# Optimization experiments

Measured on AMD Instinct MI355X. Metric: run time of the kernel, lower is better.

The kernel has to match this reference:

```python
import jax, jax.numpy as jnp
import numpy as np

DIM = 512
HEADS = 16
WS = (2, 7, 7)
N = WS[0] * WS[1] * WS[2]  # 98
NW = 64  # number of windows in mask
B_ = 512  # num_windows * batch
HEAD_DIM = DIM // HEADS
SCALE = HEAD_DIM ** -0.5
TABLE = (2 * WS[0] - 1) * (2 * WS[1] - 1) * (2 * WS[2] - 1)  # 507


def _relative_position_index():
    # Faithful to the repo (note: middle coord is NOT multiplied by (2*Ww-1),
    # matching the source exactly).
    ct, ch, cw = np.arange(WS[0]), np.arange(WS[1]), np.arange(WS[2])
    coords = np.stack(np.meshgrid(ct, ch, cw, indexing='ij'))  # [3,Th,Tw,Tw]
    flat = coords.reshape(3, -1)  # [3,N]
    rel = flat[:, :, None] - flat[:, None, :]  # [3,N,N]
    rel = rel.transpose(1, 2, 0).copy()  # [N,N,3]
    rel[:, :, 0] += WS[0] - 1
    rel[:, :, 1] += WS[1] - 1
    rel[:, :, 2] += WS[2] - 1
    rel[:, :, 0] *= (2 * WS[1] - 1) * (2 * WS[2] - 1)
    return rel.sum(-1).astype(np.int32)  # [N,N]


def setup_inputs() -> dict:
    key = jax.random.key(0)
    ks = jax.random.split(key, 7)
    x = jax.random.normal(ks[0], (B_, N, DIM), dtype=jnp.float32)
    mask = jnp.zeros((NW, N, N), dtype=jnp.float32)
    qkv_w = jax.random.normal(ks[1], (3 * DIM, DIM), dtype=jnp.float32) * (DIM ** -0.5)
    qkv_b = jnp.zeros((3 * DIM,), dtype=jnp.float32)
    proj_w = jax.random.normal(ks[2], (DIM, DIM), dtype=jnp.float32) * (DIM ** -0.5)
    proj_b = jnp.zeros((DIM,), dtype=jnp.float32)
    bias_table = jax.random.normal(ks[3], (TABLE, HEADS), dtype=jnp.float32) * 0.02
    rel_index = jnp.asarray(_relative_position_index())
    return {"x": x, "mask": mask, "qkv_w": qkv_w, "qkv_b": qkv_b,
            "proj_w": proj_w, "proj_b": proj_b, "bias_table": bias_table,
            "rel_index": rel_index}


def reference(x, mask, qkv_w, qkv_b, proj_w, proj_b, bias_table, rel_index):
    Bw, n, c = x.shape
    # QKV projection -> [3, B_, H, N, hd]
    qkv = (x @ qkv_w.T + qkv_b).reshape(Bw, n, 3, HEADS, HEAD_DIM)
    qkv = qkv.transpose(2, 0, 3, 1, 4)
    q, k, v = qkv[0], qkv[1], qkv[2]
    attn = jnp.einsum('bhnd,bhmd->bhnm', q * SCALE, k)  # [B_,H,N,N]
    # Gathered relative position bias -> [H,N,N]
    bias = bias_table[rel_index.reshape(-1)].reshape(n, n, HEADS).transpose(2, 0, 1)
    attn = attn + bias[None]
    # Broadcast mask over batch groups of nW windows
    nW = mask.shape[0]
    attn = attn.reshape(Bw // nW, nW, HEADS, n, n) + mask[None, :, None]
    attn = attn.reshape(Bw, HEADS, n, n)
    attn = jax.nn.softmax(attn, axis=-1)
    out = jnp.einsum('bhnm,bhmd->bhnd', attn, v)
    out = out.transpose(0, 2, 1, 3).reshape(Bw, n, c)
    return out @ proj_w.T + proj_b
```

## Files before the change

### kernel.cpp

```cpp
#include <hip/hip_runtime.h>
#include <stdint.h>

#define HEADS 16
#define NTOK 98
#define HD 32
#define SCALE_Q 0.17677669529663687f

typedef __attribute__((ext_vector_type(4))) float floatx4;
typedef __attribute__((ext_vector_type(8))) short shortx8;

__device__ __forceinline__ unsigned short f2bf(float f) {
  union { float f; unsigned u; } v; v.f = f;
  unsigned r = v.u + 0x7fffu + ((v.u >> 16) & 1u);
  return (unsigned short)(r >> 16);
}
__device__ __forceinline__ float bf2f(unsigned short s) {
  union { unsigned u; float f; } v; v.u = ((unsigned)s) << 16;
  return v.f;
}

__device__ __forceinline__ void gload_lds16(const void* g, void* l) {
  __builtin_amdgcn_global_load_lds(
      (const __attribute__((address_space(1))) unsigned int*)g,
      (__attribute__((address_space(3))) unsigned int*)l, 16, 0, 0);
}

__global__ void convert_x_kernel(const float* __restrict__ x,
                                 unsigned short* __restrict__ xbf) {
  int idx = blockIdx.x * 256 + threadIdx.x;
  const float4 f0 = *(const float4*)(x + (size_t)idx * 8);
  const float4 f1 = *(const float4*)(x + (size_t)idx * 8 + 4);
  union { ushort us[8]; uint4 u4; } pk;
  pk.us[0] = f2bf(f0.x); pk.us[1] = f2bf(f0.y);
  pk.us[2] = f2bf(f0.z); pk.us[3] = f2bf(f0.w);
  pk.us[4] = f2bf(f1.x); pk.us[5] = f2bf(f1.y);
  pk.us[6] = f2bf(f1.z); pk.us[7] = f2bf(f1.w);
  *(uint4*)(xbf + (size_t)idx * 8) = pk.u4;
}

__global__ void convert_w_kernel(const float* __restrict__ qkv_w,
                                 const float* __restrict__ proj_w,
                                 unsigned short* __restrict__ wq,
                                 unsigned short* __restrict__ wp) {
  int idx = blockIdx.x * 256 + threadIdx.x;
  if (idx < 1536 * 512) wq[idx] = f2bf(qkv_w[idx]);
  if (idx < 512 * 512) wp[idx] = f2bf(proj_w[idx]);
}

__global__ void bmprep_kernel(const float* __restrict__ table,
                              const int* __restrict__ rel,
                              const float* __restrict__ mask,
                              float* __restrict__ biasP,
                              float* __restrict__ maskP) {
  int idx = blockIdx.x * 256 + threadIdx.x;
  if (idx < 229376) {
    int e = idx & 31, lane = (idx >> 5) & 63;
    int rest = idx >> 11;
    int mt = rest % 7, h = rest / 7;
    int nt = e >> 2, r = e & 3;
    int i = mt * 16 + ((lane >> 4) << 2) + r;
    int j = (nt << 4) + (lane & 15);
    float v = 0.f;
    if (nt < 7 && i < NTOK && j < NTOK) v = table[rel[i * NTOK + j] * HEADS + h];
    biasP[idx] = v;
  } else {
    int t = idx - 229376;
    int e = t & 31, lane = (t >> 5) & 63;
    int rest = t >> 11;
    int mt = rest % 7, wdx = rest / 7;
    int nt = e >> 2, r = e & 3;
    int i = mt * 16 + ((lane >> 4) << 2) + r;
    int j = (nt << 4) + (lane & 15);
    float v;
    if (nt >= 7) v = 0.f;
    else if (j >= NTOK) v = -1e30f;
    else if (i >= NTOK) v = 0.f;
    else v = mask[wdx * (NTOK * NTOK) + i * NTOK + j];
    maskP[t] = v;
  }
}

__global__ __launch_bounds__(512, 2)
void qkv_gemm_kernel(const unsigned short* __restrict__ xbf,
                     const unsigned short* __restrict__ wbf,
                     const float* __restrict__ qkv_b,
                     unsigned short* __restrict__ q_out,
                     unsigned short* __restrict__ k_out,
                     unsigned short* __restrict__ v_out) {
  __shared__ unsigned short As[3][128 * 32];
  __shared__ unsigned short Bs[3][256 * 32];
  const int tid = threadIdx.x;
  const int wave = tid >> 6, lane = tid & 63;
  const int m0 = blockIdx.x * 128, n0 = blockIdx.y * 256;
  const int wm = wave & 1, wn = wave >> 1;
  const int ln15 = lane & 15, qd = lane >> 4;
  const int bl_r = lane >> 2, bl_s = lane & 3;

  const int sg_st = bl_s ^ ((bl_r >> 1) & 3);
  const int swz_rd = (qd ^ ((ln15 >> 1) & 3)) * 8;

  const unsigned short* aG = xbf + (size_t)(m0 + wave * 16 + bl_r) * 512 + sg_st * 8;
  const unsigned short* bG0 = wbf + (size_t)(n0 + wave * 32 + bl_r) * 512 + sg_st * 8;
  const unsigned short* bG1 = wbf + (size_t)(n0 + wave * 32 + 16 + bl_r) * 512 + sg_st * 8;

#define QSTAGE(bufi, kk)                                                        \
  do {                                                                          \
    gload_lds16((const void*)(aG + (kk)), (void*)&As[bufi][wave * 512]);        \
    gload_lds16((const void*)(bG0 + (kk)), (void*)&Bs[bufi][wave * 1024]);      \
    gload_lds16((const void*)(bG1 + (kk)), (void*)&Bs[bufi][wave * 1024 + 512]);\
  } while (0)

  QSTAGE(0, 0);
  QSTAGE(1, 32);

  floatx4 acc[4][4] = {};
#pragma unroll
  for (int it = 0; it < 16; ++it) {
    if (it == 15) asm volatile("s_waitcnt vmcnt(0)" ::: "memory");
    else          asm volatile("s_waitcnt vmcnt(3)" ::: "memory");
    __builtin_amdgcn_sched_barrier(0);
    __builtin_amdgcn_s_barrier();
    __builtin_amdgcn_sched_barrier(0);
    if (it + 2 < 16) QSTAGE((it + 2) % 3, (it + 2) * 32);
    const unsigned short* Ab = As[it % 3];
    const unsigned short* Bb = Bs[it % 3];
    shortx8 afrag[4], bfrag[4];
#pragma unroll
    for (int mt = 0; mt < 4; ++mt)
      afrag[mt] = *(const shortx8*)&Ab[(wm * 64 + mt * 16 + ln15) * 32 + swz_rd];
#pragma unroll
    for (int nt = 0; nt < 4; ++nt)
      bfrag[nt] = *(const shortx8*)&Bb[(wn * 64 + nt * 16 + ln15) * 32 + swz_rd];
#pragma unroll
    for (int mt = 0; mt < 4; ++mt)
#pragma unroll
      for (int nt = 0; nt < 4; ++nt)
        acc[mt][nt] = __builtin_amdgcn_mfma_f32_16x16x32_bf16(
            afrag[mt], bfrag[nt], acc[mt][nt], 0, 0, 0);
  }
#undef QSTAGE

#pragma unroll
  for (int mt = 0; mt < 4; ++mt) {
#pragma unroll
    for (int r = 0; r < 4; ++r) {
      int grow = m0 + wm * 64 + mt * 16 + qd * 4 + r;
      unsigned b = (unsigned)grow / 98u;
      unsigned i = (unsigned)grow - b * 98u;
#pragma unroll
      for (int nt = 0; nt < 4; ++nt) {
        int col = n0 + wn * 64 + nt * 16 + ln15;
        float val = acc[mt][nt][r] + qkv_b[col];
        int which = col >> 9;
        int h = (col >> 5) & 15;
        int d = col & 31;
        size_t oidx = ((size_t)(b * 16 + h) * 98 + i) * 32 + d;
        if (which == 0)      q_out[oidx] = f2bf(val * SCALE_Q);
        else if (which == 1) k_out[oidx] = f2bf(val);
        else                 v_out[oidx] = f2bf(val);
      }
    }
  }
}

__global__ __launch_bounds__(256, 4)
void attn_kernel(const unsigned short* __restrict__ qg,
                 const unsigned short* __restrict__ kg,
                 const unsigned short* __restrict__ vg,
                 const float* __restrict__ biasP,
                 const float* __restrict__ maskP,
                 unsigned short* __restrict__ outg) {
  __shared__ unsigned short Vt[32 * 136];
  __shared__ unsigned short Ps[4][16 * 40];
  const int tid = threadIdx.x;
  const int bh = blockIdx.x;
  const int b = bh >> 4, h = bh & 15, w = b & 63;
  const size_t base = (size_t)bh * (NTOK * HD);
  const int wave = tid >> 6, lane = tid & 63;
  const int ln15 = lane & 15, qd = lane >> 4;

  for (int idx = tid; idx < 544; idx += 256)
    ((uint4*)Vt)[idx] = make_uint4(0, 0, 0, 0);
  __syncthreads();
  for (int t = tid; t < 392; t += 256) {
    int i = t >> 2, seg = t & 3;
    union { uint4 u4; unsigned short us[8]; } u;
    u.u4 = *(const uint4*)(vg + base + i * 32 + seg * 8);
    int d0 = seg * 8;
#pragma unroll
    for (int e0 = 0; e0 < 8; ++e0) {
      int e = (e0 + seg * 2) & 7;
      Vt[(d0 + e) * 136 + i] = u.us[e];
    }
  }
  __syncthreads();

  floatx4 oacc[2];
#pragma unroll
  for (int mslot = 0; mslot < 2; ++mslot) {
    int mt = wave + mslot * 4;
    if (mt >= 7) break;
    const floatx4* bP = (const floatx4*)(biasP + (((size_t)h * 7 + mt) * 64 + lane) * 32);
    const floatx4* mP = (const floatx4*)(maskP + (((size_t)w * 7 + mt) * 64 + lane) * 32);
    floatx4 bb[7];
#pragma unroll
    for (int nt = 0; nt < 7; ++nt) bb[nt] = bP[nt] + mP[nt];

    shortx8 af = *(const shortx8*)(qg + base + (mt * 16 + ln15) * 32 + qd * 8);
    floatx4 sacc[7];
#pragma unroll
    for (int nt = 0; nt < 7; ++nt) {
      shortx8 bf = *(const shortx8*)(kg + base + (nt * 16 + ln15) * 32 + qd * 8);
      floatx4 z = {};
      sacc[nt] = __builtin_amdgcn_mfma_f32_16x16x32_bf16(af, bf, z, 0, 0, 0);
    }
#pragma unroll
    for (int nt = 0; nt < 7; ++nt) sacc[nt] += bb[nt];

    float linv[4];
#pragma unroll
    for (int r = 0; r < 4; ++r) {
      float mx = sacc[0][r];
#pragma unroll
      for (int nt = 1; nt < 7; ++nt) mx = fmaxf(mx, sacc[nt][r]);
#pragma unroll
      for (int off = 1; off < 16; off <<= 1)
        mx = fmaxf(mx, __shfl_xor(mx, off, 64));
      float sum = 0.f;
#pragma unroll
      for (int nt = 0; nt < 7; ++nt) {
        float p = __expf(sacc[nt][r] - mx);
        sacc[nt][r] = p;
        sum += p;
      }
#pragma unroll
      for (int off = 1; off < 16; off <<= 1) sum += __shfl_xor(sum, off, 64);
      linv[r] = 1.0f / sum;
    }
    oacc[0] = (floatx4){};
    oacc[1] = (floatx4){};
#pragma unroll
    for (int ks = 0; ks < 4; ++ks) {
#pragma unroll
      for (int nt2 = 0; nt2 < 2; ++nt2) {
        int nt = ks * 2 + nt2;
#pragma unroll
        for (int r = 0; r < 4; ++r)
          Ps[wave][(qd * 4 + r) * 40 + nt2 * 16 + ln15] = f2bf(sacc[nt][r]);
      }
      shortx8 ap = *(const shortx8*)&Ps[wave][ln15 * 40 + qd * 8];
      shortx8 bv0 = *(const shortx8*)&Vt[ln15 * 136 + ks * 32 + qd * 8];
      shortx8 bv1 = *(const shortx8*)&Vt[(16 + ln15) * 136 + ks * 32 + qd * 8];
      oacc[0] = __builtin_amdgcn_mfma_f32_16x16x32_bf16(ap, bv0, oacc[0], 0, 0, 0);
      oacc[1] = __builtin_amdgcn_mfma_f32_16x16x32_bf16(ap, bv1, oacc[1], 0, 0, 0);
    }
#pragma unroll
    for (int r = 0; r < 4; ++r) {
      int i = mt * 16 + qd * 4 + r;
      if (i < NTOK) {
        size_t ob = ((size_t)b * NTOK + i) * 512 + h * 32;
#pragma unroll
        for (int vt = 0; vt < 2; ++vt)
          outg[ob + vt * 16 + ln15] = f2bf(oacc[vt][r] * linv[r]);
      }
    }
  }
}

__global__ __launch_bounds__(512, 2)
void proj_gemm_kernel(const unsigned short* __restrict__ a,
                      const unsigned short* __restrict__ wbf,
                      const float* __restrict__ proj_b,
                      float* __restrict__ out) {
  __shared__ unsigned short As[3][128 * 32];
  __shared__ unsigned short Bs[3][256 * 32];
  const int tid = threadIdx.x;
  const int wave = tid >> 6, lane = tid & 63;
  const int m0 = blockIdx.x * 128, n0 = blockIdx.y * 256;
  const int wm = wave & 1, wn = wave >> 1;
  const int ln15 = lane & 15, qd = lane >> 4;
  const int bl_r = lane >> 2, bl_s = lane & 3;

  const int sg_st = bl_s ^ ((bl_r >> 1) & 3);
  const int swz_rd = (qd ^ ((ln15 >> 1) & 3)) * 8;

  const unsigned short* aG = a + (size_t)(m0 + wave * 16 + bl_r) * 512 + sg_st * 8;
  const unsigned short* bG0 = wbf + (size_t)(n0 + wave * 32 + bl_r) * 512 + sg_st * 8;
  const unsigned short* bG1 = wbf + (size_t)(n0 + wave * 32 + 16 + bl_r) * 512 + sg_st * 8;

#define PSTAGE(bufi, kk)                                                        \
  do {                                                                          \
    gload_lds16((const void*)(aG + (kk)), (void*)&As[bufi][wave * 512]);        \
    gload_lds16((const void*)(bG0 + (kk)), (void*)&Bs[bufi][wave * 1024]);      \
    gload_lds16((const void*)(bG1 + (kk)), (void*)&Bs[bufi][wave * 1024 + 512]);\
  } while (0)

  PSTAGE(0, 0);
  PSTAGE(1, 32);

  floatx4 acc[4][4] = {};
#pragma unroll
  for (int it = 0; it < 16; ++it) {
    if (it == 15) asm volatile("s_waitcnt vmcnt(0)" ::: "memory");
    else          asm volatile("s_waitcnt vmcnt(3)" ::: "memory");
    __builtin_amdgcn_sched_barrier(0);
    __builtin_amdgcn_s_barrier();
    __builtin_amdgcn_sched_barrier(0);
    if (it + 2 < 16) PSTAGE((it + 2) % 3, (it + 2) * 32);
    const unsigned short* Ab = As[it % 3];
    const unsigned short* Bb = Bs[it % 3];
    shortx8 afrag[4], bfrag[4];
#pragma unroll
    for (int mt = 0; mt < 4; ++mt)
      afrag[mt] = *(const shortx8*)&Ab[(wm * 64 + mt * 16 + ln15) * 32 + swz_rd];
#pragma unroll
    for (int nt = 0; nt < 4; ++nt)
      bfrag[nt] = *(const shortx8*)&Bb[(wn * 64 + nt * 16 + ln15) * 32 + swz_rd];
#pragma unroll
    for (int mt = 0; mt < 4; ++mt)
#pragma unroll
      for (int nt = 0; nt < 4; ++nt)
        acc[mt][nt] = __builtin_amdgcn_mfma_f32_16x16x32_bf16(
            afrag[mt], bfrag[nt], acc[mt][nt], 0, 0, 0);
  }
#undef PSTAGE

#pragma unroll
  for (int mt = 0; mt < 4; ++mt) {
#pragma unroll
    for (int r = 0; r < 4; ++r) {
      int grow = m0 + wm * 64 + mt * 16 + qd * 4 + r;
#pragma unroll
      for (int nt = 0; nt < 4; ++nt) {
        int col = n0 + wn * 64 + nt * 16 + ln15;
        out[(size_t)grow * 512 + col] = acc[mt][nt][r] + proj_b[col];
      }
    }
  }
}

extern "C" void kernel_launch(void* const* d_in, const int* in_sizes, int n_in,
                              void* d_out, int out_size, void* d_ws, size_t ws_size,
                              hipStream_t stream) {
  const float* x          = (const float*)d_in[0];
  const float* mask       = (const float*)d_in[1];
  const float* qkv_w      = (const float*)d_in[2];
  const float* qkv_b      = (const float*)d_in[3];
  const float* proj_w     = (const float*)d_in[4];
  const float* proj_b     = (const float*)d_in[5];
  const float* bias_table = (const float*)d_in[6];
  const int*   rel_index  = (const int*)d_in[7];
  float* out = (float*)d_out;

  char* ws = (char*)d_ws;
  unsigned short* ws_qkvw  = (unsigned short*)(ws + 0);
  unsigned short* ws_projw = (unsigned short*)(ws + 1572864);
  float*          ws_biasP = (float*)(ws + 2097152);
  float*          ws_maskP = (float*)(ws + 3014656);
  unsigned short* ws_q     = (unsigned short*)(ws + 6684672);
  unsigned short* ws_k     = (unsigned short*)(ws + 58064896);
  unsigned short* ws_v     = (unsigned short*)(ws + 109445120);
  unsigned short* ws_attn  = (unsigned short*)(ws + 160825344);
  unsigned short* ws_xbf   = ws_attn;

  hipLaunchKernelGGL(convert_x_kernel, dim3(12544), dim3(256), 0, stream,
                     x, ws_xbf);
  hipLaunchKernelGGL(convert_w_kernel, dim3(3072), dim3(256), 0, stream,
                     qkv_w, proj_w, ws_qkvw, ws_projw);
  hipLaunchKernelGGL(bmprep_kernel, dim3(4480), dim3(256), 0, stream,
                     bias_table, rel_index, mask, ws_biasP, ws_maskP);
  hipLaunchKernelGGL(qkv_gemm_kernel, dim3(392, 6), dim3(512), 0, stream,
                     ws_xbf, ws_qkvw, qkv_b, ws_q, ws_k, ws_v);
  hipLaunchKernelGGL(attn_kernel, dim3(8192), dim3(256), 0, stream,
                     ws_q, ws_k, ws_v, ws_biasP, ws_maskP, ws_attn);
  hipLaunchKernelGGL(proj_gemm_kernel, dim3(392, 2), dim3(512), 0, stream,
                     ws_attn, ws_projw, proj_b, out);
}
```

Baseline: 523.6 us.

## Store bias/mask in bf16 and use one wave per query tile in attention

The precomputed relative-position bias and window mask are now stored as bf16 instead of fp32, halving the bytes the attention kernel reads for them. The attention kernel goes from 4 to 7 waves, so each wave handles one 16-row query tile instead of looping over up to two. The whole P row block is written to shared memory once rather than staged per k-step. This trades more LDS per block and bf16 rounding of the bias and mask for fewer global reads and more parallelism per block.

```diff
diff --git a/kernel.cpp b/kernel.cpp
--- a/kernel.cpp
+++ b/kernel.cpp
@@ -50,8 +50,8 @@
 __global__ void bmprep_kernel(const float* __restrict__ table,
                               const int* __restrict__ rel,
                               const float* __restrict__ mask,
-                              float* __restrict__ biasP,
-                              float* __restrict__ maskP) {
+                              unsigned short* __restrict__ biasF,
+                              unsigned short* __restrict__ maskF) {
   int idx = blockIdx.x * 256 + threadIdx.x;
   if (idx < 229376) {
     int e = idx & 31, lane = (idx >> 5) & 63;
@@ -60,9 +60,9 @@
     int nt = e >> 2, r = e & 3;
     int i = mt * 16 + ((lane >> 4) << 2) + r;
     int j = (nt << 4) + (lane & 15);
-    float v = 0.f;
-    if (nt < 7 && i < NTOK && j < NTOK) v = table[rel[i * NTOK + j] * HEADS + h];
-    biasP[idx] = v;
+    int ii = i < NTOK ? i : 97, jj = j < NTOK ? j : 97;
+    float v = (nt < 7) ? table[rel[ii * NTOK + jj] * HEADS + h] : 0.f;
+    biasF[idx] = f2bf(v);
   } else {
     int t = idx - 229376;
     int e = t & 31, lane = (t >> 5) & 63;
@@ -74,9 +74,11 @@
     float v;
     if (nt >= 7) v = 0.f;
     else if (j >= NTOK) v = -1e30f;
-    else if (i >= NTOK) v = 0.f;
-    else v = mask[wdx * (NTOK * NTOK) + i * NTOK + j];
-    maskP[t] = v;
+    else {
+      int ii = i < NTOK ? i : 97;
+      v = mask[wdx * (NTOK * NTOK) + ii * NTOK + j];
+    }
+    maskF[t] = f2bf(v);
   }
 }
 
@@ -163,15 +165,15 @@
   }
 }
 
-__global__ __launch_bounds__(256, 4)
+__global__ __launch_bounds__(448, 6)
 void attn_kernel(const unsigned short* __restrict__ qg,
                  const unsigned short* __restrict__ kg,
                  const unsigned short* __restrict__ vg,
-                 const float* __restrict__ biasP,
-                 const float* __restrict__ maskP,
+                 const unsigned short* __restrict__ biasF,
+                 const unsigned short* __restrict__ maskF,
                  unsigned short* __restrict__ outg) {
-  __shared__ unsigned short Vt[32 * 136];
-  __shared__ unsigned short Ps[4][16 * 40];
+  __shared__ __align__(16) unsigned short Vt[32 * 136];
+  __shared__ __align__(16) unsigned short Ps[7][1928];
   const int tid = threadIdx.x;
   const int bh = blockIdx.x;
   const int b = bh >> 4, h = bh & 15, w = b & 63;
@@ -179,10 +181,12 @@
   const int wave = tid >> 6, lane = tid & 63;
   const int ln15 = lane & 15, qd = lane >> 4;
 
-  for (int idx = tid; idx < 544; idx += 256)
+  for (int idx = tid; idx < 544; idx += 448)
     ((uint4*)Vt)[idx] = make_uint4(0, 0, 0, 0);
+  for (int idx = tid; idx < 1687; idx += 448)
+    ((uint4*)Ps)[idx] = make_uint4(0, 0, 0, 0);
   __syncthreads();
-  for (int t = tid; t < 392; t += 256) {
+  for (int t = tid; t < 392; t += 448) {
     int i = t >> 2, seg = t & 3;
     union { uint4 u4; unsigned short us[8]; } u;
     u.u4 = *(const uint4*)(vg + base + i * 32 + seg * 8);
@@ -195,74 +199,74 @@
   }
   __syncthreads();
 
-  floatx4 oacc[2];
-#pragma unroll
-  for (int mslot = 0; mslot < 2; ++mslot) {
-    int mt = wave + mslot * 4;
-    if (mt >= 7) break;
-    const floatx4* bP = (const floatx4*)(biasP + (((size_t)h * 7 + mt) * 64 + lane) * 32);
-    const floatx4* mP = (const floatx4*)(maskP + (((size_t)w * 7 + mt) * 64 + lane) * 32);
-    floatx4 bb[7];
-#pragma unroll
-    for (int nt = 0; nt < 7; ++nt) bb[nt] = bP[nt] + mP[nt];
-
-    shortx8 af = *(const shortx8*)(qg + base + (mt * 16 + ln15) * 32 + qd * 8);
-    floatx4 sacc[7];
+  const int mt = wave;
+  const shortx8* bB = (const shortx8*)(biasF + (((size_t)h * 7 + mt) * 64 + lane) * 32);
+  const shortx8* mB = (const shortx8*)(maskF + (((size_t)w * 7 + mt) * 64 + lane) * 32);
+  shortx8 bias_c[4], mask_c[4];
+#pragma unroll
+  for (int c = 0; c < 4; ++c) { bias_c[c] = bB[c]; mask_c[c] = mB[c]; }
+
+  shortx8 af = *(const shortx8*)(qg + base + (mt * 16 + ln15) * 32 + qd * 8);
+  floatx4 sacc[7];
+#pragma unroll
+  for (int nt = 0; nt < 7; ++nt) {
+    shortx8 bf = *(const shortx8*)(kg + base + (nt * 16 + ln15) * 32 + qd * 8);
+    floatx4 z = {};
+    sacc[nt] = __builtin_amdgcn_mfma_f32_16x16x32_bf16(af, bf, z, 0, 0, 0);
+  }
+#pragma unroll
+  for (int nt = 0; nt < 7; ++nt)
+#pragma unroll
+    for (int r = 0; r < 4; ++r) {
+      int ee = nt * 4 + r, c = ee >> 3, el = ee & 7;
+      sacc[nt][r] += bf2f((unsigned short)bias_c[c][el]) +
+                     bf2f((unsigned short)mask_c[c][el]);
+    }
+
+  float linv[4];
+#pragma unroll
+  for (int r = 0; r < 4; ++r) {
+    float mx = sacc[0][r];
+#pragma unroll
+    for (int nt = 1; nt < 7; ++nt) mx = fmaxf(mx, sacc[nt][r]);
+#pragma unroll
+    for (int off = 1; off < 16; off <<= 1)
+      mx = fmaxf(mx, __shfl_xor(mx, off, 64));
+    float sum = 0.f;
 #pragma unroll
     for (int nt = 0; nt < 7; ++nt) {
-      shortx8 bf = *(const shortx8*)(kg + base + (nt * 16 + ln15) * 32 + qd * 8);
-      floatx4 z = {};
-      sacc[nt] = __builtin_amdgcn_mfma_f32_16x16x32_bf16(af, bf, z, 0, 0, 0);
-    }
-#pragma unroll
-    for (int nt = 0; nt < 7; ++nt) sacc[nt] += bb[nt];
-
-    float linv[4];
-#pragma unroll
-    for (int r = 0; r < 4; ++r) {
-      float mx = sacc[0][r];
-#pragma unroll
-      for (int nt = 1; nt < 7; ++nt) mx = fmaxf(mx, sacc[nt][r]);
-#pragma unroll
-      for (int off = 1; off < 16; off <<= 1)
-        mx = fmaxf(mx, __shfl_xor(mx, off, 64));
-      float sum = 0.f;
-#pragma unroll
-      for (int nt = 0; nt < 7; ++nt) {
-        float p = __expf(sacc[nt][r] - mx);
-        sacc[nt][r] = p;
-        sum += p;
-      }
-#pragma unroll
-      for (int off = 1; off < 16; off <<= 1) sum += __shfl_xor(sum, off, 64);
-      linv[r] = 1.0f / sum;
-    }
-    oacc[0] = (floatx4){};
-    oacc[1] = (floatx4){};
-#pragma unroll
-    for (int ks = 0; ks < 4; ++ks) {
-#pragma unroll
-      for (int nt2 = 0; nt2 < 2; ++nt2) {
-        int nt = ks * 2 + nt2;
-#pragma unroll
-        for (int r = 0; r < 4; ++r)
-          Ps[wave][(qd * 4 + r) * 40 + nt2 * 16 + ln15] = f2bf(sacc[nt][r]);
-      }
-      shortx8 ap = *(const shortx8*)&Ps[wave][ln15 * 40 + qd * 8];
-      shortx8 bv0 = *(const shortx8*)&Vt[ln15 * 136 + ks * 32 + qd * 8];
-      shortx8 bv1 = *(const shortx8*)&Vt[(16 + ln15) * 136 + ks * 32 + qd * 8];
-      oacc[0] = __builtin_amdgcn_mfma_f32_16x16x32_bf16(ap, bv0, oacc[0], 0, 0, 0);
-      oacc[1] = __builtin_amdgcn_mfma_f32_16x16x32_bf16(ap, bv1, oacc[1], 0, 0, 0);
-    }
-#pragma unroll
-    for (int r = 0; r < 4; ++r) {
-      int i = mt * 16 + qd * 4 + r;
-      if (i < NTOK) {
-        size_t ob = ((size_t)b * NTOK + i) * 512 + h * 32;
-#pragma unroll
-        for (int vt = 0; vt < 2; ++vt)
-          outg[ob + vt * 16 + ln15] = f2bf(oacc[vt][r] * linv[r]);
-      }
+      float p = __expf(sacc[nt][r] - mx);
+      sacc[nt][r] = p;
+      sum += p;
+    }
+#pragma unroll
+    for (int off = 1; off < 16; off <<= 1) sum += __shfl_xor(sum, off, 64);
+    linv[r] = 1.0f / sum;
+  }
+
+  unsigned short* Pw = Ps[wave];
+#pragma unroll
+  for (int nt = 0; nt < 7; ++nt)
+#pragma unroll
+    for (int r = 0; r < 4; ++r)
+      Pw[(qd * 4 + r) * 120 + nt * 16 + ln15] = f2bf(sacc[nt][r]);
+
+  floatx4 o0 = {}, o1 = {};
+#pragma unroll
+  for (int ks = 0; ks < 4; ++ks) {
+    shortx8 ap = *(const shortx8*)&Pw[ln15 * 120 + ks * 32 + qd * 8];
+    shortx8 bv0 = *(const shortx8*)&Vt[ln15 * 136 + ks * 32 + qd * 8];
+    shortx8 bv1 = *(const shortx8*)&Vt[(16 + ln15) * 136 + ks * 32 + qd * 8];
+    o0 = __builtin_amdgcn_mfma_f32_16x16x32_bf16(ap, bv0, o0, 0, 0, 0);
+    o1 = __builtin_amdgcn_mfma_f32_16x16x32_bf16(ap, bv1, o1, 0, 0, 0);
+  }
+#pragma unroll
+  for (int r = 0; r < 4; ++r) {
+    int i = mt * 16 + qd * 4 + r;
+    if (i < NTOK) {
+      size_t ob = ((size_t)b * NTOK + i) * 512 + h * 32;
+      outg[ob + ln15] = f2bf(o0[r] * linv[r]);
+      outg[ob + 16 + ln15] = f2bf(o1[r] * linv[r]);
     }
   }
 }
@@ -355,12 +359,12 @@
   char* ws = (char*)d_ws;
   unsigned short* ws_qkvw  = (unsigned short*)(ws + 0);
   unsigned short* ws_projw = (unsigned short*)(ws + 1572864);
-  float*          ws_biasP = (float*)(ws + 2097152);
-  float*          ws_maskP = (float*)(ws + 3014656);
-  unsigned short* ws_q     = (unsigned short*)(ws + 6684672);
-  unsigned short* ws_k     = (unsigned short*)(ws + 58064896);
-  unsigned short* ws_v     = (unsigned short*)(ws + 109445120);
-  unsigned short* ws_attn  = (unsigned short*)(ws + 160825344);
+  unsigned short* ws_biasF = (unsigned short*)(ws + 2097152);
+  unsigned short* ws_maskF = (unsigned short*)(ws + 2555904);
+  unsigned short* ws_q     = (unsigned short*)(ws + 4390912);
+  unsigned short* ws_k     = (unsigned short*)(ws + 55771136);
+  unsigned short* ws_v     = (unsigned short*)(ws + 107151360);
+  unsigned short* ws_attn  = (unsigned short*)(ws + 158531584);
   unsigned short* ws_xbf   = ws_attn;
 
   hipLaunchKernelGGL(convert_x_kernel, dim3(12544), dim3(256), 0, stream,
@@ -368,11 +372,11 @@
   hipLaunchKernelGGL(convert_w_kernel, dim3(3072), dim3(256), 0, stream,
                      qkv_w, proj_w, ws_qkvw, ws_projw);
   hipLaunchKernelGGL(bmprep_kernel, dim3(4480), dim3(256), 0, stream,
-                     bias_table, rel_index, mask, ws_biasP, ws_maskP);
+                     bias_table, rel_index, mask, ws_biasF, ws_maskF);
   hipLaunchKernelGGL(qkv_gemm_kernel, dim3(392, 6), dim3(512), 0, stream,
                      ws_xbf, ws_qkvw, qkv_b, ws_q, ws_k, ws_v);
-  hipLaunchKernelGGL(attn_kernel, dim3(8192), dim3(256), 0, stream,
-                     ws_q, ws_k, ws_v, ws_biasP, ws_maskP, ws_attn);
+  hipLaunchKernelGGL(attn_kernel, dim3(8192), dim3(448), 0, stream,
+                     ws_q, ws_k, ws_v, ws_biasF, ws_maskF, ws_attn);
   hipLaunchKernelGGL(proj_gemm_kernel, dim3(392, 2), dim3(512), 0, stream,
                      ws_attn, ws_projw, proj_b, out);
 }
```

Result: faster. 452.8 us (-13.5%).
